# Kernel optimization log

Hardware: AMD Instinct MI355X
Metric: run time of the kernel (lower is better)

## Reference

```python
import jax, jax.numpy as jnp
import numpy as np
import math

BLOCK = 32
TAU = 0.1
INIT_SPARSITY = 0.1


def setup_inputs() -> dict:
    key = jax.random.key(0)
    k1, k2, k3, k4 = jax.random.split(key, 4)
    B, S, D_IN, D_OUT = 4, 2048, 4096, 4096
    x = jax.random.normal(k1, (B, S, D_IN), dtype=jnp.float32)
    # nn.Linear default init: uniform(-1/sqrt(in), 1/sqrt(in))
    bound = 1.0 / math.sqrt(D_IN)
    weight = jax.random.uniform(k2, (D_OUT, D_IN), minval=-bound, maxval=bound, dtype=jnp.float32)
    bias = jax.random.uniform(k3, (D_OUT,), minval=-bound, maxval=bound, dtype=jnp.float32)
    # scores init per _init_scores: randn*0.1 + logit(init_sparsity)
    target_logit = math.log(INIT_SPARSITY / (1.0 - INIT_SPARSITY))
    scores = jax.random.normal(k4, (D_OUT // BLOCK, D_IN // BLOCK), dtype=jnp.float32) * 0.1 + target_logit
    return {"x": x, "weight": weight, "bias": bias, "scores": scores}


def reference(x, weight, bias, scores):
    # block mask: sigmoid(scores) > tau, expanded 32x32 per block
    block_mask = (jax.nn.sigmoid(scores) > TAU).astype(weight.dtype)  # [O/32, I/32]
    full_mask = jnp.repeat(jnp.repeat(block_mask, BLOCK, axis=0), BLOCK, axis=1)  # [O, I]
    pruned_weight = weight * full_mask
    # F.linear: x @ W^T + b
    return jnp.einsum('bsi,oi->bso', x, pruned_weight) + bias
```

## Files before the change

### kernel.cpp

```cpp
#include <hip/hip_runtime.h>


#define BM 128
#define BN 128
#define BK 64

typedef __attribute__((ext_vector_type(8))) short bf16x8;
typedef __attribute__((ext_vector_type(4))) float f32x4;

__device__ __forceinline__ unsigned short f2bf(float f) {
    union { float f; unsigned u; } v; v.f = f;
    return (unsigned short)((v.u + 0x7FFFu + ((v.u >> 16) & 1u)) >> 16);
}

#define THRESH (-2.1972245773362196f)

__global__ __launch_bounds__(256)
void prep(const float* __restrict__ X, const float* __restrict__ W,
          const float* __restrict__ scores,
          unsigned short* __restrict__ Xb, unsigned short* __restrict__ Wb,
          unsigned long long* __restrict__ mbits,
          int M, int N, int K) {
    const int b   = blockIdx.x;
    const int tid = threadIdx.x;
    const int KBlk = K >> 5;

    if (b < 2048) {
        for (int row = b; row < M; row += 2048) {
            const float* src = X + (long)row * K;
            unsigned short* dst = Xb + (long)row * K;
            for (int k = tid * 4; k < K; k += 1024) {
                const float4 a = *(const float4*)(src + k);
                ushort4 p;
                p.x = f2bf(a.x); p.y = f2bf(a.y); p.z = f2bf(a.z); p.w = f2bf(a.w);
                *(ushort4*)(dst + k) = p;
            }
        }
    } else if (b < 3072) {
        for (int row = b - 2048; row < N; row += 1024) {
            const float* src = W + (long)row * K;
            unsigned short* dst = Wb + (long)row * K;
            const float* srow = scores + (long)(row >> 5) * KBlk;
            for (int k = tid * 4; k < K; k += 1024) {
                if (srow[k >> 5] > THRESH) {
                    const float4 a = *(const float4*)(src + k);
                    ushort4 p;
                    p.x = f2bf(a.x); p.y = f2bf(a.y); p.z = f2bf(a.z); p.w = f2bf(a.w);
                    *(ushort4*)(dst + k) = p;
                }
            }
        }
    } else {
        const int nb = (b - 3072) * 4 + (tid >> 6);
        const int l  = tid & 63;
        const unsigned long long b0 = __ballot(scores[(long)nb * KBlk + l] > THRESH);
        const unsigned long long b1 = __ballot(scores[(long)nb * KBlk + 64 + l] > THRESH);
        if (l == 0) { mbits[nb * 2] = b0; mbits[nb * 2 + 1] = b1; }
    }
}


__device__ __forceinline__ unsigned long long rfl64(unsigned long long v) {
    unsigned lo = __builtin_amdgcn_readfirstlane((unsigned)v);
    unsigned hi = __builtin_amdgcn_readfirstlane((unsigned)(v >> 32));
    return ((unsigned long long)hi << 32) | lo;
}

#define GLL16(g, l) __builtin_amdgcn_global_load_lds( \
    (const __attribute__((address_space(1))) void*)(g), \
    (__attribute__((address_space(3))) void*)(l), 16, 0, 0)

#define PB(i, s) ((unsigned)((((s) & 32) ? mhi[i] : mlo[i]) >> (2 * ((s) & 31))) & 3)

#define STAGE(sAbuf, sBbuf, ko, q0, q1, q2, q3) do { \
    const char* b0_ = (q0) ? gB : gA; \
    const char* b1_ = (q1) ? gB : gA; \
    const char* b2_ = (q2) ? gB : gA; \
    const char* b3_ = (q3) ? gB : gA; \
    GLL16(gA  + 0L * 32 * K2 + (ko), (sAbuf) + 0 * 4096 + ldso); \
    GLL16(gA  + 1L * 32 * K2 + (ko), (sAbuf) + 1 * 4096 + ldso); \
    GLL16(gA  + 2L * 32 * K2 + (ko), (sAbuf) + 2 * 4096 + ldso); \
    GLL16(gA  + 3L * 32 * K2 + (ko), (sAbuf) + 3 * 4096 + ldso); \
    GLL16(b0_ + 0L * 32 * K2 + (ko), (sBbuf) + 0 * 4096 + ldso); \
    GLL16(b1_ + 1L * 32 * K2 + (ko), (sBbuf) + 1 * 4096 + ldso); \
    GLL16(b2_ + 2L * 32 * K2 + (ko), (sBbuf) + 2 * 4096 + ldso); \
    GLL16(b3_ + 3L * 32 * K2 + (ko), (sBbuf) + 3 * 4096 + ldso); \
} while (0)

__global__ __launch_bounds__(256)
void mpl_main(const unsigned short* __restrict__ Xb,
              const unsigned short* __restrict__ Wb,
              const float* __restrict__ bias,
              const unsigned long long* __restrict__ mb,
              float* __restrict__ out, int M, int N, int K)
{
    __shared__ unsigned short sA0[BM * BK];
    __shared__ unsigned short sB0[BN * BK];
    __shared__ unsigned short sA1[BM * BK];
    __shared__ unsigned short sB1[BN * BK];

    const int tid  = threadIdx.x;
    const int lane = tid & 63;
    const int wave = tid >> 6;
    const int m0   = blockIdx.y * BM;
    const int n0   = blockIdx.x * BN;
    const int wm   = (wave & 1) * 64;
    const int wn   = (wave >> 1) * 64;
    const long K2  = (long)K * 2;

    const int nbb = n0 >> 5;
    unsigned long long mlo[4], mhi[4];
#pragma unroll
    for (int i = 0; i < 4; i++) {
        mlo[i] = rfl64(mb[(nbb + i) * 2]);
        mhi[i] = rfl64(mb[(nbb + i) * 2 + 1]);
    }

    f32x4 acc[4][4];
#pragma unroll
    for (int i = 0; i < 4; i++)
#pragma unroll
        for (int j = 0; j < 4; j++)
            acc[i][j] = (f32x4){0.f, 0.f, 0.f, 0.f};

    const int r8   = tid >> 3;
    const int cswz = ((tid & 7) ^ ((tid >> 3) & 7)) * 16;
    const char* gA = (const char*)Xb + (long)(m0 + r8) * K2 + cswz;
    const char* gB = (const char*)Wb + (long)(n0 + r8) * K2 + cswz;
    char* sA0c = (char*)sA0;
    char* sB0c = (char*)sB0;
    char* sA1c = (char*)sA1;
    char* sB1c = (char*)sB1;
    const int ldso = wave * 1024;

    const int fr   = lane & 15;
    const int cxor = lane & 7;
    const int kqc  = lane >> 4;
    const int rowA = wm + fr;
    const int rowB = wn + fr;

    unsigned p0 = PB(0, 0), p1 = PB(1, 0), p2 = PB(2, 0), p3 = PB(3, 0);
    STAGE(sA0c, sB0c, 0L, p0, p1, p2, p3);

#pragma unroll 2
    for (int s = 0; s < 64; ++s) {
        const unsigned c0 = p0, c1 = p1, c2 = p2, c3 = p3;
        if (s < 63) {
            p0 = PB(0, s + 1); p1 = PB(1, s + 1); p2 = PB(2, s + 1); p3 = PB(3, s + 1);
            const long konext = (long)(s + 1) * 128;
            if (s & 1) STAGE(sA0c, sB0c, konext, p0, p1, p2, p3);
            else       STAGE(sA1c, sB1c, konext, p0, p1, p2, p3);
            asm volatile("s_waitcnt vmcnt(8)" ::: "memory");
        } else {
            asm volatile("s_waitcnt vmcnt(0)" ::: "memory");
        }
        __builtin_amdgcn_s_barrier();
        __builtin_amdgcn_sched_barrier(0);

        const char* cA = (s & 1) ? sA1c : sA0c;
        const char* cB = (s & 1) ? sB1c : sB0c;

        const unsigned plo = (wave >> 1) ? c2 : c0;
        const unsigned phi = (wave >> 1) ? c3 : c1;

        if (plo | phi) {
#pragma unroll
            for (int kbl = 0; kbl < 2; ++kbl) {
                if (!(((plo | phi) >> kbl) & 1)) continue;
                const int boff = ((kqc | (kbl << 2)) ^ cxor) * 16;

                bf16x8 af[4];
#pragma unroll
                for (int mi = 0; mi < 4; mi++)
                    af[mi] = *(const bf16x8*)(cA + (rowA + mi * 16) * 128 + boff);

                if ((plo >> kbl) & 1) {
                    const bf16x8 bf0 = *(const bf16x8*)(cB + (rowB + 0)  * 128 + boff);
                    const bf16x8 bf1 = *(const bf16x8*)(cB + (rowB + 16) * 128 + boff);
#pragma unroll
                    for (int mi = 0; mi < 4; mi++) {
                        acc[mi][0] = __builtin_amdgcn_mfma_f32_16x16x32_bf16(af[mi], bf0, acc[mi][0], 0, 0, 0);
                        acc[mi][1] = __builtin_amdgcn_mfma_f32_16x16x32_bf16(af[mi], bf1, acc[mi][1], 0, 0, 0);
                    }
                }
                if ((phi >> kbl) & 1) {
                    const bf16x8 bf2 = *(const bf16x8*)(cB + (rowB + 32) * 128 + boff);
                    const bf16x8 bf3 = *(const bf16x8*)(cB + (rowB + 48) * 128 + boff);
#pragma unroll
                    for (int mi = 0; mi < 4; mi++) {
                        acc[mi][2] = __builtin_amdgcn_mfma_f32_16x16x32_bf16(af[mi], bf2, acc[mi][2], 0, 0, 0);
                        acc[mi][3] = __builtin_amdgcn_mfma_f32_16x16x32_bf16(af[mi], bf3, acc[mi][3], 0, 0, 0);
                    }
                }
            }
        }
        __builtin_amdgcn_sched_barrier(0);
        __builtin_amdgcn_s_barrier();
    }

    const int cn = lane & 15;
    const int rq = (lane >> 4) * 4;
#pragma unroll
    for (int ni = 0; ni < 4; ni++) {
        const int n = n0 + wn + ni * 16 + cn;
        const float b = bias[n];
#pragma unroll
        for (int mi = 0; mi < 4; mi++) {
#pragma unroll
            for (int r = 0; r < 4; r++) {
                const int m = m0 + wm + mi * 16 + rq + r;
                out[(long)m * N + n] = acc[mi][ni][r] + b;
            }
        }
    }
}


#define FBK 32
#define LDSS (FBK + 8)
__global__ __launch_bounds__(256, 2)
void mpl_gemm_fb(const float* __restrict__ X, const float* __restrict__ W,
                 const float* __restrict__ bias, const float* __restrict__ scores,
                 float* __restrict__ out, int M, int N, int K)
{
    __shared__ unsigned short sA[BM * LDSS];
    __shared__ unsigned short sB[BN * LDSS];
    const int tid = threadIdx.x;
    const int m0 = blockIdx.y * BM, n0 = blockIdx.x * BN;
    const int wave = tid >> 6, lane = tid & 63;
    const int wm = (wave & 1) * 64, wn = (wave >> 1) * 64;
    const int kblocks = K >> 5;
    f32x4 acc[4][4];
#pragma unroll
    for (int i = 0; i < 4; i++)
#pragma unroll
        for (int j = 0; j < 4; j++) acc[i][j] = (f32x4){0.f,0.f,0.f,0.f};
    int srow[4], sc4[4], snb[4];
#pragma unroll
    for (int i = 0; i < 4; i++) {
        int f = tid + 256 * i;
        srow[i] = f >> 3; sc4[i] = f & 7; snb[i] = (n0 + srow[i]) >> 5;
    }
    for (int k0 = 0; k0 < K; k0 += FBK) {
        const int kb = k0 >> 5;
#pragma unroll
        for (int i = 0; i < 4; i++) {
            const float4 v = *(const float4*)(X + (long)(m0 + srow[i]) * K + k0 + sc4[i] * 4);
            ushort4 p; p.x = f2bf(v.x); p.y = f2bf(v.y); p.z = f2bf(v.z); p.w = f2bf(v.w);
            *(ushort4*)&sA[srow[i] * LDSS + sc4[i] * 4] = p;
        }
#pragma unroll
        for (int i = 0; i < 4; i++) {
            const float msk = (scores[snb[i] * kblocks + kb] > THRESH) ? 1.0f : 0.0f;
            const float4 v = *(const float4*)(W + (long)(n0 + srow[i]) * K + k0 + sc4[i] * 4);
            ushort4 p; p.x = f2bf(v.x*msk); p.y = f2bf(v.y*msk); p.z = f2bf(v.z*msk); p.w = f2bf(v.w*msk);
            *(ushort4*)&sB[srow[i] * LDSS + sc4[i] * 4] = p;
        }
        __syncthreads();
        const int fr = lane & 15, kq = (lane >> 4) * 8;
        bf16x8 af[4], bfr[4];
#pragma unroll
        for (int mi = 0; mi < 4; mi++) af[mi] = *(const bf16x8*)&sA[(wm + mi*16 + fr) * LDSS + kq];
#pragma unroll
        for (int ni = 0; ni < 4; ni++) bfr[ni] = *(const bf16x8*)&sB[(wn + ni*16 + fr) * LDSS + kq];
#pragma unroll
        for (int mi = 0; mi < 4; mi++)
#pragma unroll
            for (int ni = 0; ni < 4; ni++)
                acc[mi][ni] = __builtin_amdgcn_mfma_f32_16x16x32_bf16(af[mi], bfr[ni], acc[mi][ni], 0,0,0);
        __syncthreads();
    }
    const int cn = lane & 15, rq = (lane >> 4) * 4;
#pragma unroll
    for (int ni = 0; ni < 4; ni++) {
        const int n = n0 + wn + ni * 16 + cn;
        const float b = bias[n];
#pragma unroll
        for (int mi = 0; mi < 4; mi++)
#pragma unroll
            for (int r = 0; r < 4; r++)
                out[(long)(m0 + wm + mi*16 + rq + r) * N + n] = acc[mi][ni][r] + b;
    }
}

extern "C" void kernel_launch(void* const* d_in, const int* in_sizes, int n_in,
                              void* d_out, int out_size, void* d_ws, size_t ws_size,
                              hipStream_t stream) {
    const float* X      = (const float*)d_in[0];
    const float* W      = (const float*)d_in[1];
    const float* bias   = (const float*)d_in[2];
    const float* scores = (const float*)d_in[3];
    float* out          = (float*)d_out;

    const int N = in_sizes[2];
    const int K = in_sizes[1] / N;
    const int M = in_sizes[0] / K;
    const int KB = K >> 5;
    const int NB = N >> 5;

    const size_t mk2 = (size_t)M * K * 2;
    const size_t nk2 = (size_t)N * K * 2;
    const size_t need = mk2 + nk2 + (size_t)NB * 16;

    if (ws_size >= need && KB == 128 && (M % 128) == 0 && (N % 128) == 0 &&
        (K % 1024) == 0 && (NB % 4) == 0) {
        unsigned short* Xb = (unsigned short*)d_ws;
        unsigned short* Wb = (unsigned short*)((char*)d_ws + mk2);
        unsigned long long* mbits = (unsigned long long*)((char*)d_ws + mk2 + nk2);

        prep<<<3072 + NB / 4, 256, 0, stream>>>(X, W, scores, Xb, Wb, mbits, M, N, K);

        dim3 grid(N / BN, M / BM);
        mpl_main<<<grid, dim3(256), 0, stream>>>(Xb, Wb, bias, mbits, out, M, N, K);
    } else {
        dim3 grid(N / BN, M / BM);
        mpl_gemm_fb<<<grid, dim3(256), 0, stream>>>(X, W, bias, scores, out, M, N, K);
    }
}
```

Before: 549.3 us.

## Replace 128x128 GEMM with 256x256 two-phase 8-wave pipelined kernel

```diff
diff --git a/kernel.cpp b/kernel.cpp
--- a/kernel.cpp
+++ b/kernel.cpp
@@ -1,9 +1,5 @@
 #include <hip/hip_runtime.h>
 
-
-#define BM 128
-#define BN 128
-#define BK 64
 
 typedef __attribute__((ext_vector_type(8))) short bf16x8;
 typedef __attribute__((ext_vector_type(4))) float f32x4;
@@ -70,131 +66,144 @@
     (const __attribute__((address_space(1))) void*)(g), \
     (__attribute__((address_space(3))) void*)(l), 16, 0, 0)
 
-#define PB(i, s) ((unsigned)((((s) & 32) ? mhi[i] : mlo[i]) >> (2 * ((s) & 31))) & 3)
-
-#define STAGE(sAbuf, sBbuf, ko, q0, q1, q2, q3) do { \
-    const char* b0_ = (q0) ? gB : gA; \
-    const char* b1_ = (q1) ? gB : gA; \
-    const char* b2_ = (q2) ? gB : gA; \
-    const char* b3_ = (q3) ? gB : gA; \
-    GLL16(gA  + 0L * 32 * K2 + (ko), (sAbuf) + 0 * 4096 + ldso); \
-    GLL16(gA  + 1L * 32 * K2 + (ko), (sAbuf) + 1 * 4096 + ldso); \
-    GLL16(gA  + 2L * 32 * K2 + (ko), (sAbuf) + 2 * 4096 + ldso); \
-    GLL16(gA  + 3L * 32 * K2 + (ko), (sAbuf) + 3 * 4096 + ldso); \
-    GLL16(b0_ + 0L * 32 * K2 + (ko), (sBbuf) + 0 * 4096 + ldso); \
-    GLL16(b1_ + 1L * 32 * K2 + (ko), (sBbuf) + 1 * 4096 + ldso); \
-    GLL16(b2_ + 2L * 32 * K2 + (ko), (sBbuf) + 2 * 4096 + ldso); \
-    GLL16(b3_ + 3L * 32 * K2 + (ko), (sBbuf) + 3 * 4096 + ldso); \
-} while (0)
-
-__global__ __launch_bounds__(256)
-void mpl_main(const unsigned short* __restrict__ Xb,
-              const unsigned short* __restrict__ Wb,
-              const float* __restrict__ bias,
-              const unsigned long long* __restrict__ mb,
-              float* __restrict__ out, int M, int N, int K)
+#define PB2(np, t) ((unsigned)((((t) & 32) ? ((np) ? w1hi : w0hi) : ((np) ? w1lo : w0lo)) \
+                               >> (2 * ((t) & 31))) & 3u)
+
+#define ARD(BO, MH, i, kk) (*(const bf16x8*)(lds + (BO) + ((MH) << 14) + \
+    (arb + (i) * 16 + fr) * 128 + ((((kq) | ((kk) << 2)) ^ cx) << 4)))
+#define BRD(BO, np, j, kk) (*(const bf16x8*)(lds + (BO) + bkb + \
+    (brb + ((np) * 2 + (j)) * 16 + fr) * 128 + ((((kq) | ((kk) << 2)) ^ cx) << 4)))
+
+#define MFMAS(MH) \
+    if (pa & 1u) { _Pragma("unroll") for (int i = 0; i < 4; ++i) { \
+        acc[(MH)*4+i][0] = __builtin_amdgcn_mfma_f32_16x16x32_bf16(a0[i], b0[0], acc[(MH)*4+i][0], 0,0,0); \
+        acc[(MH)*4+i][1] = __builtin_amdgcn_mfma_f32_16x16x32_bf16(a0[i], b0[1], acc[(MH)*4+i][1], 0,0,0); } } \
+    if (pb & 1u) { _Pragma("unroll") for (int i = 0; i < 4; ++i) { \
+        acc[(MH)*4+i][2] = __builtin_amdgcn_mfma_f32_16x16x32_bf16(a0[i], b0[2], acc[(MH)*4+i][2], 0,0,0); \
+        acc[(MH)*4+i][3] = __builtin_amdgcn_mfma_f32_16x16x32_bf16(a0[i], b0[3], acc[(MH)*4+i][3], 0,0,0); } } \
+    if (pa & 2u) { _Pragma("unroll") for (int i = 0; i < 4; ++i) { \
+        acc[(MH)*4+i][0] = __builtin_amdgcn_mfma_f32_16x16x32_bf16(a1[i], b1[0], acc[(MH)*4+i][0], 0,0,0); \
+        acc[(MH)*4+i][1] = __builtin_amdgcn_mfma_f32_16x16x32_bf16(a1[i], b1[1], acc[(MH)*4+i][1], 0,0,0); } } \
+    if (pb & 2u) { _Pragma("unroll") for (int i = 0; i < 4; ++i) { \
+        acc[(MH)*4+i][2] = __builtin_amdgcn_mfma_f32_16x16x32_bf16(a1[i], b1[2], acc[(MH)*4+i][2], 0,0,0); \
+        acc[(MH)*4+i][3] = __builtin_amdgcn_mfma_f32_16x16x32_bf16(a1[i], b1[3], acc[(MH)*4+i][3], 0,0,0); } }
+
+__global__ __launch_bounds__(512, 2)
+void mpl_2ph(const unsigned short* __restrict__ Xb,
+             const unsigned short* __restrict__ Wb,
+             const float* __restrict__ bias,
+             const unsigned long long* __restrict__ mb,
+             float* __restrict__ out, int M, int N, int K)
 {
-    __shared__ unsigned short sA0[BM * BK];
-    __shared__ unsigned short sB0[BN * BK];
-    __shared__ unsigned short sA1[BM * BK];
-    __shared__ unsigned short sB1[BN * BK];
+    extern __shared__ __attribute__((aligned(16))) char lds[];
 
     const int tid  = threadIdx.x;
     const int lane = tid & 63;
     const int wave = tid >> 6;
-    const int m0   = blockIdx.y * BM;
-    const int n0   = blockIdx.x * BN;
-    const int wm   = (wave & 1) * 64;
-    const int wn   = (wave >> 1) * 64;
+    const int n0   = blockIdx.x * 256;
+    const int m0   = blockIdx.y * 256;
     const long K2  = (long)K * 2;
-
-    const int nbb = n0 >> 5;
-    unsigned long long mlo[4], mhi[4];
-#pragma unroll
-    for (int i = 0; i < 4; i++) {
-        mlo[i] = rfl64(mb[(nbb + i) * 2]);
-        mhi[i] = rfl64(mb[(nbb + i) * 2 + 1]);
-    }
-
-    f32x4 acc[4][4];
-#pragma unroll
-    for (int i = 0; i < 4; i++)
+    const int NT   = K >> 6;
+
+    const int wm = (wave >> 2) * 128;
+    const int wn = (wave & 3) * 64;
+
+    const int nbw = (n0 >> 5) + (wave & 3) * 2;
+    const unsigned long long w0lo = rfl64(mb[nbw * 2]);
+    const unsigned long long w0hi = rfl64(mb[nbw * 2 + 1]);
+    const unsigned long long w1lo = rfl64(mb[(nbw + 1) * 2]);
+    const unsigned long long w1hi = rfl64(mb[(nbw + 1) * 2 + 1]);
+
+    f32x4 acc[8][4];
+#pragma unroll
+    for (int i = 0; i < 8; i++)
 #pragma unroll
         for (int j = 0; j < 4; j++)
             acc[i][j] = (f32x4){0.f, 0.f, 0.f, 0.f};
 
-    const int r8   = tid >> 3;
-    const int cswz = ((tid & 7) ^ ((tid >> 3) & 7)) * 16;
-    const char* gA = (const char*)Xb + (long)(m0 + r8) * K2 + cswz;
-    const char* gB = (const char*)Wb + (long)(n0 + r8) * K2 + cswz;
-    char* sA0c = (char*)sA0;
-    char* sB0c = (char*)sB0;
-    char* sA1c = (char*)sA1;
-    char* sB1c = (char*)sB1;
+    const int r0   = wave * 8 + (lane >> 3);
+    const int cswz = ((lane & 7) ^ (lane >> 3)) * 16;
+    const char* gA = (const char*)Xb + (long)(m0 + r0) * K2 + cswz;
+    const char* gB = (const char*)Wb + (long)(n0 + r0) * K2 + cswz;
     const int ldso = wave * 1024;
 
-    const int fr   = lane & 15;
-    const int cxor = lane & 7;
-    const int kqc  = lane >> 4;
-    const int rowA = wm + fr;
-    const int rowB = wn + fr;
-
-    unsigned p0 = PB(0, 0), p1 = PB(1, 0), p2 = PB(2, 0), p3 = PB(3, 0);
-    STAGE(sA0c, sB0c, 0L, p0, p1, p2, p3);
-
-#pragma unroll 2
-    for (int s = 0; s < 64; ++s) {
-        const unsigned c0 = p0, c1 = p1, c2 = p2, c3 = p3;
-        if (s < 63) {
-            p0 = PB(0, s + 1); p1 = PB(1, s + 1); p2 = PB(2, s + 1); p3 = PB(3, s + 1);
-            const long konext = (long)(s + 1) * 128;
-            if (s & 1) STAGE(sA0c, sB0c, konext, p0, p1, p2, p3);
-            else       STAGE(sA1c, sB1c, konext, p0, p1, p2, p3);
-            asm volatile("s_waitcnt vmcnt(8)" ::: "memory");
+    auto STAGEH = [&](int h) {
+        const int t = h >> 2, kind = h & 3;
+        char* l = lds + ((t & 1) << 16) + (kind << 14) + ldso;
+        const long kbyte = (long)t * 128;
+        if (kind < 2) {
+            const char* g = gA + (long)(kind * 64) * K2 + kbyte;
+            GLL16(g, l);
+            GLL16(g + 128 * K2, l + 8192);
         } else {
-            asm volatile("s_waitcnt vmcnt(0)" ::: "memory");
-        }
+            const char* g = gB + (long)((kind & 1) * 128) * K2 + kbyte;
+            GLL16(g, l);
+            GLL16(g + 64 * K2, l + 8192);
+        }
+    };
+
+    const int fr  = lane & 15;
+    const int kq  = lane >> 4;
+    const int cx  = lane & 7;
+    const int arb = (wave >> 2) * 64;
+    const int bkb = 32768 + ((wave & 3) >> 1) * 16384;
+    const int brb = (wave & 1) * 64;
+
+    STAGEH(0); STAGEH(1); STAGEH(2); STAGEH(3);
+    STAGEH(4); STAGEH(6); STAGEH(7);
+    asm volatile("s_waitcnt vmcnt(6)" ::: "memory");
+    __builtin_amdgcn_s_barrier();
+
+    for (int t = 0; t < NT; ++t) {
+        const int bo = (t & 1) << 16;
+        const unsigned pa = PB2(0, t), pb = PB2(1, t);
+        const unsigned anyk = pa | pb;
+        bf16x8 a0[4], a1[4], b0[4], b1[4];
+
+        if (anyk & 1u) {
+#pragma unroll
+            for (int i = 0; i < 4; ++i) a0[i] = ARD(bo, 0, i, 0);
+        }
+        if (anyk & 2u) {
+#pragma unroll
+            for (int i = 0; i < 4; ++i) a1[i] = ARD(bo, 0, i, 1);
+        }
+        if (pa & 1u) { b0[0] = BRD(bo, 0, 0, 0); b0[1] = BRD(bo, 0, 1, 0); }
+        if (pa & 2u) { b1[0] = BRD(bo, 0, 0, 1); b1[1] = BRD(bo, 0, 1, 1); }
+        if (pb & 1u) { b0[2] = BRD(bo, 1, 0, 0); b0[3] = BRD(bo, 1, 1, 0); }
+        if (pb & 2u) { b1[2] = BRD(bo, 1, 0, 1); b1[3] = BRD(bo, 1, 1, 1); }
+        if (t + 1 < NT) STAGEH(4 * (t + 1) + 1);
+        if (t < NT - 1) asm volatile("s_waitcnt vmcnt(8)" ::: "memory");
+        else            asm volatile("s_waitcnt vmcnt(0)" ::: "memory");
         __builtin_amdgcn_s_barrier();
+        asm volatile("s_waitcnt lgkmcnt(0)" ::: "memory");
         __builtin_amdgcn_sched_barrier(0);
-
-        const char* cA = (s & 1) ? sA1c : sA0c;
-        const char* cB = (s & 1) ? sB1c : sB0c;
-
-        const unsigned plo = (wave >> 1) ? c2 : c0;
-        const unsigned phi = (wave >> 1) ? c3 : c1;
-
-        if (plo | phi) {
-#pragma unroll
-            for (int kbl = 0; kbl < 2; ++kbl) {
-                if (!(((plo | phi) >> kbl) & 1)) continue;
-                const int boff = ((kqc | (kbl << 2)) ^ cxor) * 16;
-
-                bf16x8 af[4];
-#pragma unroll
-                for (int mi = 0; mi < 4; mi++)
-                    af[mi] = *(const bf16x8*)(cA + (rowA + mi * 16) * 128 + boff);
-
-                if ((plo >> kbl) & 1) {
-                    const bf16x8 bf0 = *(const bf16x8*)(cB + (rowB + 0)  * 128 + boff);
-                    const bf16x8 bf1 = *(const bf16x8*)(cB + (rowB + 16) * 128 + boff);
-#pragma unroll
-                    for (int mi = 0; mi < 4; mi++) {
-                        acc[mi][0] = __builtin_amdgcn_mfma_f32_16x16x32_bf16(af[mi], bf0, acc[mi][0], 0, 0, 0);
-                        acc[mi][1] = __builtin_amdgcn_mfma_f32_16x16x32_bf16(af[mi], bf1, acc[mi][1], 0, 0, 0);
-                    }
-                }
-                if ((phi >> kbl) & 1) {
-                    const bf16x8 bf2 = *(const bf16x8*)(cB + (rowB + 32) * 128 + boff);
-                    const bf16x8 bf3 = *(const bf16x8*)(cB + (rowB + 48) * 128 + boff);
-#pragma unroll
-                    for (int mi = 0; mi < 4; mi++) {
-                        acc[mi][2] = __builtin_amdgcn_mfma_f32_16x16x32_bf16(af[mi], bf2, acc[mi][2], 0, 0, 0);
-                        acc[mi][3] = __builtin_amdgcn_mfma_f32_16x16x32_bf16(af[mi], bf3, acc[mi][3], 0, 0, 0);
-                    }
-                }
-            }
-        }
+        __builtin_amdgcn_s_setprio(1);
+        MFMAS(0)
+        __builtin_amdgcn_s_setprio(0);
+        __builtin_amdgcn_s_barrier();
+
+        if (anyk & 1u) {
+#pragma unroll
+            for (int i = 0; i < 4; ++i) a0[i] = ARD(bo, 1, i, 0);
+        }
+        if (anyk & 2u) {
+#pragma unroll
+            for (int i = 0; i < 4; ++i) a1[i] = ARD(bo, 1, i, 1);
+        }
+        if (t + 2 < NT) {
+            STAGEH(4 * (t + 2) + 0);
+            STAGEH(4 * (t + 2) + 2);
+            STAGEH(4 * (t + 2) + 3);
+        }
+        if (t < NT - 2)      asm volatile("s_waitcnt vmcnt(8)" ::: "memory");
+        else if (t == NT - 2) asm volatile("s_waitcnt vmcnt(2)" ::: "memory");
+        __builtin_amdgcn_s_barrier();
+        asm volatile("s_waitcnt lgkmcnt(0)" ::: "memory");
         __builtin_amdgcn_sched_barrier(0);
+        __builtin_amdgcn_s_setprio(1);
+        MFMAS(1)
+        __builtin_amdgcn_s_setprio(0);
         __builtin_amdgcn_s_barrier();
     }
 
@@ -203,19 +212,21 @@
 #pragma unroll
     for (int ni = 0; ni < 4; ni++) {
         const int n = n0 + wn + ni * 16 + cn;
-        const float b = bias[n];
-#pragma unroll
-        for (int mi = 0; mi < 4; mi++) {
+        const float bv = bias[n];
+#pragma unroll
+        for (int mi = 0; mi < 8; mi++) {
 #pragma unroll
             for (int r = 0; r < 4; r++) {
                 const int m = m0 + wm + mi * 16 + rq + r;
-                out[(long)m * N + n] = acc[mi][ni][r] + b;
+                out[(long)m * N + n] = acc[mi][ni][r] + bv;
             }
         }
     }
 }
 
 
+#define FBM 128
+#define FBN 128
 #define FBK 32
 #define LDSS (FBK + 8)
 __global__ __launch_bounds__(256, 2)
@@ -223,10 +234,10 @@
                  const float* __restrict__ bias, const float* __restrict__ scores,
                  float* __restrict__ out, int M, int N, int K)
 {
-    __shared__ unsigned short sA[BM * LDSS];
-    __shared__ unsigned short sB[BN * LDSS];
+    __shared__ unsigned short sA[FBM * LDSS];
+    __shared__ unsigned short sB[FBN * LDSS];
     const int tid = threadIdx.x;
-    const int m0 = blockIdx.y * BM, n0 = blockIdx.x * BN;
+    const int m0 = blockIdx.y * FBM, n0 = blockIdx.x * FBN;
     const int wave = tid >> 6, lane = tid & 63;
     const int wm = (wave & 1) * 64, wn = (wave >> 1) * 64;
     const int kblocks = K >> 5;
@@ -234,7 +245,7 @@
 #pragma unroll
     for (int i = 0; i < 4; i++)
 #pragma unroll
-        for (int j = 0; j < 4; j++) acc[i][j] = (f32x4){0.f,0.f,0.f,0.f};
+        for (int j = 0; j < 4; j++) acc[i][j] = (f32x4){0.f, 0.f, 0.f, 0.f};
     int srow[4], sc4[4], snb[4];
 #pragma unroll
     for (int i = 0; i < 4; i++) {
@@ -257,17 +268,17 @@
             *(ushort4*)&sB[srow[i] * LDSS + sc4[i] * 4] = p;
         }
         __syncthreads();
-        const int fr = lane & 15, kq = (lane >> 4) * 8;
+        const int fr = lane & 15, kqf = (lane >> 4) * 8;
         bf16x8 af[4], bfr[4];
 #pragma unroll
-        for (int mi = 0; mi < 4; mi++) af[mi] = *(const bf16x8*)&sA[(wm + mi*16 + fr) * LDSS + kq];
-#pragma unroll
-        for (int ni = 0; ni < 4; ni++) bfr[ni] = *(const bf16x8*)&sB[(wn + ni*16 + fr) * LDSS + kq];
+        for (int mi = 0; mi < 4; mi++) af[mi] = *(const bf16x8*)&sA[(wm + mi*16 + fr) * LDSS + kqf];
+#pragma unroll
+        for (int ni = 0; ni < 4; ni++) bfr[ni] = *(const bf16x8*)&sB[(wn + ni*16 + fr) * LDSS + kqf];
 #pragma unroll
         for (int mi = 0; mi < 4; mi++)
 #pragma unroll
             for (int ni = 0; ni < 4; ni++)
-                acc[mi][ni] = __builtin_amdgcn_mfma_f32_16x16x32_bf16(af[mi], bfr[ni], acc[mi][ni], 0,0,0);
+                acc[mi][ni] = __builtin_amdgcn_mfma_f32_16x16x32_bf16(af[mi], bfr[ni], acc[mi][ni], 0, 0, 0);
         __syncthreads();
     }
     const int cn = lane & 15, rq = (lane >> 4) * 4;
@@ -302,18 +313,25 @@
     const size_t nk2 = (size_t)N * K * 2;
     const size_t need = mk2 + nk2 + (size_t)NB * 16;
 
-    if (ws_size >= need && KB == 128 && (M % 128) == 0 && (N % 128) == 0 &&
-        (K % 1024) == 0 && (NB % 4) == 0) {
+    if (ws_size >= need && KB == 128 && (M % 256) == 0 && (N % 256) == 0 &&
+        (K % 1024) == 0 && (K >> 6) >= 3 && (NB % 4) == 0) {
         unsigned short* Xb = (unsigned short*)d_ws;
         unsigned short* Wb = (unsigned short*)((char*)d_ws + mk2);
         unsigned long long* mbits = (unsigned long long*)((char*)d_ws + mk2 + nk2);
 
+        static int attr_set = 0;
+        if (!attr_set) {
+            hipFuncSetAttribute(reinterpret_cast<const void*>(mpl_2ph),
+                                hipFuncAttributeMaxDynamicSharedMemorySize, 131072);
+            attr_set = 1;
+        }
+
         prep<<<3072 + NB / 4, 256, 0, stream>>>(X, W, scores, Xb, Wb, mbits, M, N, K);
 
-        dim3 grid(N / BN, M / BM);
-        mpl_main<<<grid, dim3(256), 0, stream>>>(Xb, Wb, bias, mbits, out, M, N, K);
+        dim3 grid(N / 256, M / 256);
+        mpl_2ph<<<grid, dim3(512), 131072, stream>>>(Xb, Wb, bias, mbits, out, M, N, K);
     } else {
-        dim3 grid(N / BN, M / BM);
+        dim3 grid(N / FBN, M / FBM);
         mpl_gemm_fb<<<grid, dim3(256), 0, stream>>>(X, W, bias, scores, out, M, N, K);
     }
 }
```

Result: faster. 502.3 us (-8.6%).
